# Kernel tuning notes

Measured on AMD Instinct MI355X. Metric: run time of the kernel, lower is better.

## Reference

```python
import jax, jax.numpy as jnp
import numpy as np

B, C, D_IN, D_H, D_OUT = 131072, 16, 256, 1024, 256


def setup_inputs() -> dict:
    key = jax.random.key(0)
    k = jax.random.split(key, 6)
    return {
        "x": jax.random.normal(k[0], (B, D_IN), dtype=jnp.float32),
        "cat_ids": jax.random.randint(k[1], (B,), 0, C, dtype=jnp.int32),
        "W1": jax.random.normal(k[2], (C, D_IN, D_H), dtype=jnp.float32) * (1.0 / np.sqrt(D_IN)),
        "b1": jax.random.normal(k[3], (C, D_H), dtype=jnp.float32) * 0.02,
        "W2": jax.random.normal(k[4], (C, D_H, D_OUT), dtype=jnp.float32) * (1.0 / np.sqrt(D_H)),
        "b2": jax.random.normal(k[5], (C, D_OUT), dtype=jnp.float32) * 0.02,
    }


def _routed_linear(x, cat_ids, W, b):
    # Category-routed linear: out[i] = x[i] @ W[cat_ids[i]] + b[cat_ids[i]].
    # Loop over the small fixed category count (not over tokens); each branch
    # is a dense GEMM masked by the routing assignment. This is equivalent to
    # the original gather -> per-category Linear -> scatter/argsort pattern
    # without materializing per-token weight gathers.
    num_categories = W.shape[0]
    out = jnp.zeros((x.shape[0], W.shape[2]), dtype=x.dtype)
    for c in range(num_categories):
        mask = (cat_ids == c)[:, None]
        out = out + jnp.where(mask, x @ W[c] + b[c], jnp.zeros((), x.dtype))
    return out


def reference(x, cat_ids, W1, b1, W2, b2):
    hidden = jax.nn.relu(_routed_linear(x, cat_ids, W1, b1))
    return _routed_linear(hidden, cat_ids, W2, b2)
```

## Files before the change

kernel.cpp:

```cpp
#include <hip/hip_runtime.h>
#include <hip/hip_bf16.h>

#define BB   131072
#define CC   16
#define DIN  256
#define DH   1024
#define DOUT 256
#define TM   128
#define NHB  16
#define NB   512

typedef __attribute__((ext_vector_type(8))) short bf16x8;
typedef __attribute__((ext_vector_type(4))) short short4v;
typedef __attribute__((ext_vector_type(4))) float f32x4;

__device__ inline unsigned short f2b(float f) {
  union { float f; unsigned u; } v; v.f = f;
  unsigned u = v.u;
  return (unsigned short)((u + 0x7fffu + ((u >> 16) & 1u)) >> 16);
}

__device__ inline void gload_lds16(const void* g, void* l) {
  __builtin_amdgcn_global_load_lds(
      (const __attribute__((address_space(1))) void*)g,
      (__attribute__((address_space(3))) void*)l, 16, 0, 0);
}

#define MFMA16(a, b, c) __builtin_amdgcn_mfma_f32_16x16x32_bf16((a), (b), (c), 0, 0, 0)

__global__ void hist_k(const int* __restrict__ cat, int* __restrict__ blockhist) {
  __shared__ int h[CC];
  const int tid = threadIdx.x;
  if (tid < CC) h[tid] = 0;
  __syncthreads();
  const int i = blockIdx.x * 256 + tid;
  atomicAdd(&h[cat[i]], 1);
  __syncthreads();
  if (tid < CC) blockhist[blockIdx.x * CC + tid] = h[tid];
}

__global__ void offsets2_k(const int* __restrict__ blockhist,
                           int* __restrict__ counts, int* __restrict__ padoff,
                           int* __restrict__ base) {
  __shared__ int part[CC][64];
  __shared__ int pref[CC][64];
  __shared__ int scnt[CC];
  __shared__ int spad[CC + 1];
  const int tid = threadIdx.x;
  const int c = tid >> 6;
  const int g = tid & 63;
  int h[8];
  int s = 0;
#pragma unroll
  for (int i = 0; i < 8; i++) {
    h[i] = blockhist[(g * 8 + i) * CC + c];
    s += h[i];
  }
  part[c][g] = s;
  __syncthreads();
  if (g == 0) {
    int r = 0;
    for (int j = 0; j < 64; j++) { pref[c][j] = r; r += part[c][j]; }
    scnt[c] = r;
  }
  __syncthreads();
  if (tid == 0) {
    int acc = 0;
    for (int c2 = 0; c2 < CC; c2++) {
      spad[c2] = acc;
      padoff[c2] = acc;
      counts[c2] = scnt[c2];
      acc += ((scnt[c2] + TM - 1) / TM) * TM;
    }
    spad[CC] = acc;
    padoff[CC] = acc;
  }
  __syncthreads();
  int run = spad[c] + pref[c][g];
#pragma unroll
  for (int i = 0; i < 8; i++) {
    base[(g * 8 + i) * CC + c] = run;
    run += h[i];
  }
}

__global__ void scatter2_k(const int* __restrict__ cat, const int* __restrict__ base,
                           int* __restrict__ idx) {
  __shared__ int cur[CC];
  const int tid = threadIdx.x;
  if (tid < CC) cur[tid] = base[blockIdx.x * CC + tid];
  __syncthreads();
  const int i = blockIdx.x * 256 + tid;
  const int c = cat[i];
  const int pos = atomicAdd(&cur[c], 1);
  idx[pos] = i;
}

__global__ void conv_w1_k(const float* __restrict__ W1, short* __restrict__ w1b) {
  int t = blockIdx.x * blockDim.x + threadIdx.x;
  int n  = t & 1023;
  int j8 = (t >> 10) & 31;
  int c  = t >> 15;
  const float* src = W1 + (size_t)c * DIN * DH;
  bf16x8 o;
#pragma unroll
  for (int i = 0; i < 8; i++)
    o[i] = (short)f2b(src[(size_t)(j8 * 8 + i) * DH + n]);
  char* dst = (char*)w1b + (size_t)c * 524288
            + (n >> 6) * 32768 + ((n >> 4) & 3) * 8192 + (j8 >> 2) * 1024
            + ((n & 15) + 16 * (j8 & 3)) * 16;
  *(bf16x8*)dst = o;
}

__global__ void conv_w2_k(const float* __restrict__ W2, short* __restrict__ w2b) {
  int t = blockIdx.x * blockDim.x + threadIdx.x;
  int n  = t & 255;
  int j8 = (t >> 8) & 127;
  int c  = t >> 15;
  const float* src = W2 + (size_t)c * DH * DOUT;
  bf16x8 o;
#pragma unroll
  for (int i = 0; i < 8; i++)
    o[i] = (short)f2b(src[(size_t)(j8 * 8 + i) * DOUT + n]);
  char* dst = (char*)w2b + (size_t)c * 524288
            + (j8 >> 3) * 32768 + (n >> 4) * 2048 + ((j8 >> 2) & 1) * 1024
            + ((n & 15) + 16 * (j8 & 3)) * 16;
  *(bf16x8*)dst = o;
}

#define W2OFF  65536
#define HSOFF  131072
#define TKOFF  147456
#define B1OFF  147968
#define B2OFF  152064
#define SMSZ   153088

__launch_bounds__(512, 2)
__global__ void mlp_k(const float* __restrict__ x,
                      const float* __restrict__ b1,
                      const float* __restrict__ b2,
                      const short* __restrict__ w1b,
                      const short* __restrict__ w2b,
                      const int* __restrict__ idx,
                      const int* __restrict__ padoff,
                      const int* __restrict__ counts,
                      float* __restrict__ out) {
  __shared__ __align__(16) char sm[SMSZ];

  const int bhw = blockIdx.x;
  const int wg = (bhw & 7) * 130 + (bhw >> 3);
  const int p = wg * TM;
  const int total = padoff[CC];
  if (p >= total) return;
  int c = 0;
  while (padoff[c + 1] <= p) c++;
  const int cnt = counts[c];
  const int start = p - padoff[c];

  const int tid  = threadIdx.x;
  const int lane = tid & 63;
  const int w    = tid >> 6;
  const int wt   = w >> 1;
  const int wh   = w & 1;
  const int lrow = lane & 15;
  const int lgrp = lane >> 4;

  char*  hsb   = sm + HSOFF;
  int*   toksp = (int*)(sm + TKOFF);
  float* b1s   = (float*)(sm + B1OFF);
  float* b2s   = (float*)(sm + B2OFF);

  {
    const int r = tid >> 2;
    const int q = tid & 3;
    const int pos = start + r;
    int tok = (pos < cnt) ? idx[p + r] : -1;
    if (q == 0) toksp[r] = tok;
    char* tb = sm + (r >> 4) * 8192 + (r & 15) * 16;
    if (tok >= 0) {
      const f32x4* src = (const f32x4*)(x + (size_t)tok * DIN) + q * 16;
#pragma unroll
      for (int t = 0; t < 8; t++) {
        f32x4 v0 = src[2 * t];
        f32x4 v1 = src[2 * t + 1];
        bf16x8 o;
        o[0] = (short)f2b(v0[0]); o[1] = (short)f2b(v0[1]);
        o[2] = (short)f2b(v0[2]); o[3] = (short)f2b(v0[3]);
        o[4] = (short)f2b(v1[0]); o[5] = (short)f2b(v1[1]);
        o[6] = (short)f2b(v1[2]); o[7] = (short)f2b(v1[3]);
        *(bf16x8*)(tb + (2 * q + (t >> 2)) * 1024 + (t & 3) * 256) = o;
      }
    } else {
      bf16x8 z = {0, 0, 0, 0, 0, 0, 0, 0};
#pragma unroll
      for (int t = 0; t < 8; t++)
        *(bf16x8*)(tb + (2 * q + (t >> 2)) * 1024 + (t & 3) * 256) = z;
    }
    if (tid < 256) ((f32x4*)b1s)[tid] = ((const f32x4*)(b1 + (size_t)c * DH))[tid];
    if (tid < 64)  ((f32x4*)b2s)[tid] = ((const f32x4*)(b2 + (size_t)c * DOUT))[tid];
  }
  __syncthreads();

  bf16x8 xf[2][8];
#pragma unroll
  for (int ti = 0; ti < 2; ti++)
#pragma unroll
    for (int ks = 0; ks < 8; ks++)
      xf[ti][ks] = *(const bf16x8*)(sm + (2 * wt + ti) * 8192 + ks * 1024 + lane * 16);
  __syncthreads();

  const char* w1g = (const char*)w1b + (size_t)c * 524288;
  const char* w2g = (const char*)w2b + (size_t)c * 524288;

  auto stage1 = [&](int i) {
    const char* src = w1g + (size_t)i * 32768;
    char* dst = sm + (i & 1) * 32768;
#pragma unroll
    for (int j = 0; j < 4; j++) {
      int chunk = (w * 4 + j) * 1024;
      gload_lds16(src + chunk + lane * 16, dst + chunk);
    }
  };
  auto stage2 = [&](int i) {
    const char* src = w2g + (size_t)i * 32768;
    char* dst = sm + W2OFF + (i & 1) * 32768;
#pragma unroll
    for (int j = 0; j < 4; j++) {
      int chunk = (w * 4 + j) * 1024;
      gload_lds16(src + chunk + lane * 16, dst + chunk);
    }
  };

  stage1(0);
  stage2(0);
  asm volatile("s_waitcnt vmcnt(0)" ::: "memory");
  __syncthreads();

  f32x4 acc2[2][8];
#pragma unroll
  for (int ti = 0; ti < 2; ti++)
#pragma unroll
    for (int ni = 0; ni < 8; ni++)
      acc2[ti][ni] = (f32x4){0.f, 0.f, 0.f, 0.f};

  for (int hb = 0; hb < NHB; hb++) {
    const char* w1c = sm + (hb & 1) * 32768;
    const char* w2c = sm + W2OFF + (hb & 1) * 32768;

    if (hb < NHB - 1) { stage1(hb + 1); stage2(hb + 1); }

    f32x4 acc1[2][2];
#pragma unroll
    for (int ti = 0; ti < 2; ti++)
#pragma unroll
      for (int nj = 0; nj < 2; nj++)
        acc1[ti][nj] = (f32x4){0.f, 0.f, 0.f, 0.f};

#pragma unroll
    for (int ks = 0; ks < 8; ks++) {
      bf16x8 a0 = *(const bf16x8*)(w1c + (2 * wh + 0) * 8192 + ks * 1024 + lane * 16);
      bf16x8 a1 = *(const bf16x8*)(w1c + (2 * wh + 1) * 8192 + ks * 1024 + lane * 16);
      acc1[0][0] = MFMA16(a0, xf[0][ks], acc1[0][0]);
      acc1[1][0] = MFMA16(a0, xf[1][ks], acc1[1][0]);
      acc1[0][1] = MFMA16(a1, xf[0][ks], acc1[0][1]);
      acc1[1][1] = MFMA16(a1, xf[1][ks], acc1[1][1]);
    }

#pragma unroll
    for (int nj = 0; nj < 2; nj++) {
      f32x4 bv = *(const f32x4*)(b1s + hb * 64 + (2 * wh + nj) * 16 + lgrp * 4);
#pragma unroll
      for (int ti = 0; ti < 2; ti++) {
        short4v h;
#pragma unroll
        for (int jj = 0; jj < 4; jj++)
          h[jj] = (short)f2b(fmaxf(acc1[ti][nj][jj] + bv[jj], 0.0f));
        *(short4v*)(hsb + (2 * wt + ti) * 2048 + wh * 1024
                    + (lrow + 16 * (2 * nj + (lgrp >> 1))) * 16 + (lgrp & 1) * 8) = h;
      }
    }
    if (hb < NHB - 1)
      asm volatile("s_waitcnt vmcnt(8) lgkmcnt(0)" ::: "memory");
    else
      asm volatile("s_waitcnt vmcnt(0) lgkmcnt(0)" ::: "memory");
    __builtin_amdgcn_s_barrier();

#pragma unroll
    for (int ks = 0; ks < 2; ks++) {
      bf16x8 hf0 = *(const bf16x8*)(hsb + (2 * wt + 0) * 2048 + ks * 1024 + lane * 16);
      bf16x8 hf1 = *(const bf16x8*)(hsb + (2 * wt + 1) * 2048 + ks * 1024 + lane * 16);
#pragma unroll
      for (int ni = 0; ni < 8; ni++) {
        bf16x8 a2 = *(const bf16x8*)(w2c + (wh * 8 + ni) * 2048 + ks * 1024 + lane * 16);
        acc2[0][ni] = MFMA16(a2, hf0, acc2[0][ni]);
        acc2[1][ni] = MFMA16(a2, hf1, acc2[1][ni]);
      }
    }
    asm volatile("s_waitcnt vmcnt(4) lgkmcnt(0)" ::: "memory");
    __builtin_amdgcn_s_barrier();
  }

#pragma unroll
  for (int ti = 0; ti < 2; ti++) {
    const int tok = toksp[(2 * wt + ti) * 16 + lrow];
    if (tok >= 0) {
#pragma unroll
      for (int ni = 0; ni < 8; ni++) {
        const int n0 = (wh * 8 + ni) * 16 + lgrp * 4;
        f32x4 bv = *(const f32x4*)(b2s + n0);
        f32x4 v = acc2[ti][ni] + bv;
        *(f32x4*)(out + (size_t)tok * DOUT + n0) = v;
      }
    }
  }
}

extern "C" void kernel_launch(void* const* d_in, const int* in_sizes, int n_in,
                              void* d_out, int out_size, void* d_ws, size_t ws_size,
                              hipStream_t stream) {
  (void)in_sizes; (void)n_in; (void)out_size; (void)ws_size;
  const float* x   = (const float*)d_in[0];
  const int*   cat = (const int*)d_in[1];
  const float* W1  = (const float*)d_in[2];
  const float* b1  = (const float*)d_in[3];
  const float* W2  = (const float*)d_in[4];
  const float* b2  = (const float*)d_in[5];
  float* out = (float*)d_out;

  char* ws = (char*)d_ws;
  int* counts    = (int*)(ws);
  int* padoff    = (int*)(ws + 128);
  int* blockhist = (int*)(ws + 4096);
  int* base      = (int*)(ws + 65536);
  int* idx       = (int*)(ws + 131072);
  short* w1b     = (short*)(ws + (1 << 20));
  short* w2b     = (short*)(ws + (1 << 20) + 8388608);

  hist_k<<<NB, 256, 0, stream>>>(cat, blockhist);
  offsets2_k<<<1, 1024, 0, stream>>>(blockhist, counts, padoff, base);
  scatter2_k<<<NB, 256, 0, stream>>>(cat, base, idx);
  conv_w1_k<<<2048, 256, 0, stream>>>(W1, w1b);
  conv_w2_k<<<2048, 256, 0, stream>>>(W2, w2b);

  const int ntiles = BB / TM + CC;
  mlp_k<<<ntiles, 512, 0, stream>>>(x, b1, b2, w1b, w2b, idx, padoff, counts, out);
}
```

Measured before the change: 243.8 us.

## Split hidden-block loop into barrier-separated phases with prefetch-all-then-MFMA and setprio

Restructures each hidden-block iteration into four phases. Each phase first issues all its LDS fragment reads (and one of the global->LDS stage copies), then hits a block barrier, and then runs a dense MFMA burst under raised wave priority. This is a ping-pong style schedule meant to keep waves in lockstep so LDS reads and matrix-core work from different waves interleave better. It adds many extra barriers and more live registers for the prefetched fragments, which risks sync stalls and lower occupancy. The stage1/stage2 prefetches are also spread across phases rather than issued together.

Result: slower. 264.6 us (+8.6%).

```diff
diff --git a/kernel.cpp b/kernel.cpp
--- a/kernel.cpp
+++ b/kernel.cpp
@@ -246,8 +246,7 @@
   for (int hb = 0; hb < NHB; hb++) {
     const char* w1c = sm + (hb & 1) * 32768;
     const char* w2c = sm + W2OFF + (hb & 1) * 32768;
-
-    if (hb < NHB - 1) { stage1(hb + 1); stage2(hb + 1); }
+    const bool notlast = (hb < NHB - 1);
 
     f32x4 acc1[2][2];
 #pragma unroll
@@ -256,48 +255,102 @@
       for (int nj = 0; nj < 2; nj++)
         acc1[ti][nj] = (f32x4){0.f, 0.f, 0.f, 0.f};
 
-#pragma unroll
-    for (int ks = 0; ks < 8; ks++) {
-      bf16x8 a0 = *(const bf16x8*)(w1c + (2 * wh + 0) * 8192 + ks * 1024 + lane * 16);
-      bf16x8 a1 = *(const bf16x8*)(w1c + (2 * wh + 1) * 8192 + ks * 1024 + lane * 16);
-      acc1[0][0] = MFMA16(a0, xf[0][ks], acc1[0][0]);
-      acc1[1][0] = MFMA16(a0, xf[1][ks], acc1[1][0]);
-      acc1[0][1] = MFMA16(a1, xf[0][ks], acc1[0][1]);
-      acc1[1][1] = MFMA16(a1, xf[1][ks], acc1[1][1]);
-    }
-
-#pragma unroll
-    for (int nj = 0; nj < 2; nj++) {
-      f32x4 bv = *(const f32x4*)(b1s + hb * 64 + (2 * wh + nj) * 16 + lgrp * 4);
-#pragma unroll
-      for (int ti = 0; ti < 2; ti++) {
-        short4v h;
-#pragma unroll
-        for (int jj = 0; jj < 4; jj++)
-          h[jj] = (short)f2b(fmaxf(acc1[ti][nj][jj] + bv[jj], 0.0f));
-        *(short4v*)(hsb + (2 * wt + ti) * 2048 + wh * 1024
-                    + (lrow + 16 * (2 * nj + (lgrp >> 1))) * 16 + (lgrp & 1) * 8) = h;
-      }
-    }
-    if (hb < NHB - 1)
-      asm volatile("s_waitcnt vmcnt(8) lgkmcnt(0)" ::: "memory");
-    else
-      asm volatile("s_waitcnt vmcnt(0) lgkmcnt(0)" ::: "memory");
-    __builtin_amdgcn_s_barrier();
-
-#pragma unroll
-    for (int ks = 0; ks < 2; ks++) {
-      bf16x8 hf0 = *(const bf16x8*)(hsb + (2 * wt + 0) * 2048 + ks * 1024 + lane * 16);
-      bf16x8 hf1 = *(const bf16x8*)(hsb + (2 * wt + 1) * 2048 + ks * 1024 + lane * 16);
+    {
+      bf16x8 a[8];
+#pragma unroll
+      for (int ks = 0; ks < 8; ks++)
+        a[ks] = *(const bf16x8*)(w1c + (2 * wh) * 8192 + ks * 1024 + lane * 16);
+      if (notlast) stage1(hb + 1);
+      __builtin_amdgcn_s_barrier();
+      asm volatile("s_waitcnt lgkmcnt(0)" ::: "memory");
+      __builtin_amdgcn_sched_barrier(0);
+      __builtin_amdgcn_s_setprio(1);
+#pragma unroll
+      for (int ks = 0; ks < 8; ks++) {
+        acc1[0][0] = MFMA16(a[ks], xf[0][ks], acc1[0][0]);
+        acc1[1][0] = MFMA16(a[ks], xf[1][ks], acc1[1][0]);
+      }
+      __builtin_amdgcn_s_setprio(0);
+      __builtin_amdgcn_s_barrier();
+    }
+
+    {
+      bf16x8 a[8];
+#pragma unroll
+      for (int ks = 0; ks < 8; ks++)
+        a[ks] = *(const bf16x8*)(w1c + (2 * wh + 1) * 8192 + ks * 1024 + lane * 16);
+      if (notlast) stage2(hb + 1);
+      __builtin_amdgcn_s_barrier();
+      asm volatile("s_waitcnt lgkmcnt(0)" ::: "memory");
+      __builtin_amdgcn_sched_barrier(0);
+      __builtin_amdgcn_s_setprio(1);
+#pragma unroll
+      for (int ks = 0; ks < 8; ks++) {
+        acc1[0][1] = MFMA16(a[ks], xf[0][ks], acc1[0][1]);
+        acc1[1][1] = MFMA16(a[ks], xf[1][ks], acc1[1][1]);
+      }
+      __builtin_amdgcn_s_setprio(0);
+#pragma unroll
+      for (int nj = 0; nj < 2; nj++) {
+        f32x4 bv = *(const f32x4*)(b1s + hb * 64 + (2 * wh + nj) * 16 + lgrp * 4);
+#pragma unroll
+        for (int ti = 0; ti < 2; ti++) {
+          short4v h;
+#pragma unroll
+          for (int jj = 0; jj < 4; jj++)
+            h[jj] = (short)f2b(fmaxf(acc1[ti][nj][jj] + bv[jj], 0.0f));
+          *(short4v*)(hsb + (2 * wt + ti) * 2048 + wh * 1024
+                      + (lrow + 16 * (2 * nj + (lgrp >> 1))) * 16 + (lgrp & 1) * 8) = h;
+        }
+      }
+      if (notlast)
+        asm volatile("s_waitcnt vmcnt(8) lgkmcnt(0)" ::: "memory");
+      else
+        asm volatile("s_waitcnt vmcnt(0) lgkmcnt(0)" ::: "memory");
+      __builtin_amdgcn_s_barrier();
+    }
+
+    {
+      bf16x8 hf0 = *(const bf16x8*)(hsb + (2 * wt + 0) * 2048 + lane * 16);
+      bf16x8 hf1 = *(const bf16x8*)(hsb + (2 * wt + 1) * 2048 + lane * 16);
+      bf16x8 a2[8];
+#pragma unroll
+      for (int ni = 0; ni < 8; ni++)
+        a2[ni] = *(const bf16x8*)(w2c + (wh * 8 + ni) * 2048 + lane * 16);
+      __builtin_amdgcn_s_barrier();
+      asm volatile("s_waitcnt lgkmcnt(0)" ::: "memory");
+      __builtin_amdgcn_sched_barrier(0);
+      __builtin_amdgcn_s_setprio(1);
 #pragma unroll
       for (int ni = 0; ni < 8; ni++) {
-        bf16x8 a2 = *(const bf16x8*)(w2c + (wh * 8 + ni) * 2048 + ks * 1024 + lane * 16);
-        acc2[0][ni] = MFMA16(a2, hf0, acc2[0][ni]);
-        acc2[1][ni] = MFMA16(a2, hf1, acc2[1][ni]);
-      }
-    }
-    asm volatile("s_waitcnt vmcnt(4) lgkmcnt(0)" ::: "memory");
-    __builtin_amdgcn_s_barrier();
+        acc2[0][ni] = MFMA16(a2[ni], hf0, acc2[0][ni]);
+        acc2[1][ni] = MFMA16(a2[ni], hf1, acc2[1][ni]);
+      }
+      __builtin_amdgcn_s_setprio(0);
+      __builtin_amdgcn_s_barrier();
+    }
+
+    {
+      bf16x8 hf0 = *(const bf16x8*)(hsb + (2 * wt + 0) * 2048 + 1024 + lane * 16);
+      bf16x8 hf1 = *(const bf16x8*)(hsb + (2 * wt + 1) * 2048 + 1024 + lane * 16);
+      bf16x8 a2[8];
+#pragma unroll
+      for (int ni = 0; ni < 8; ni++)
+        a2[ni] = *(const bf16x8*)(w2c + (wh * 8 + ni) * 2048 + 1024 + lane * 16);
+      __builtin_amdgcn_s_barrier();
+      asm volatile("s_waitcnt lgkmcnt(0)" ::: "memory");
+      __builtin_amdgcn_sched_barrier(0);
+      __builtin_amdgcn_s_setprio(1);
+#pragma unroll
+      for (int ni = 0; ni < 8; ni++) {
+        acc2[0][ni] = MFMA16(a2[ni], hf0, acc2[0][ni]);
+        acc2[1][ni] = MFMA16(a2[ni], hf1, acc2[1][ni]);
+      }
+      __builtin_amdgcn_s_setprio(0);
+      if (notlast)
+        asm volatile("s_waitcnt vmcnt(4)" ::: "memory");
+      __builtin_amdgcn_s_barrier();
+    }
   }
 
 #pragma unroll
```

## Software-pipeline hidden blocks with halved chunk size and double-buffered hidden tile

Applied to the files above, without the earlier changes.

Halves the hidden-dimension chunk (32 hidden units per step instead of 64) and relayouts W1/W2 bf16 buffers to match, shrinking LDS use. Restructures the loop so the second GEMM for chunk i-1 overlaps with the first GEMM for chunk i, using a double-buffered hidden tile. This removes one barrier per iteration and raises MFMA priority. In exchange there are twice as many iterations and barriers, and each iteration waits on vmcnt(0), so prefetch latency may be exposed.

After: 243.7 us. Within noise of the previous version (-0.0%).

```diff
diff --git a/kernel.cpp b/kernel.cpp
--- a/kernel.cpp
+++ b/kernel.cpp
@@ -7,7 +7,7 @@
 #define DH   1024
 #define DOUT 256
 #define TM   128
-#define NHB  16
+#define NHB  32
 #define NB   512
 
 typedef __attribute__((ext_vector_type(8))) short bf16x8;
@@ -107,7 +107,7 @@
   for (int i = 0; i < 8; i++)
     o[i] = (short)f2b(src[(size_t)(j8 * 8 + i) * DH + n]);
   char* dst = (char*)w1b + (size_t)c * 524288
-            + (n >> 6) * 32768 + ((n >> 4) & 3) * 8192 + (j8 >> 2) * 1024
+            + (n >> 5) * 16384 + ((n >> 4) & 1) * 8192 + (j8 >> 2) * 1024
             + ((n & 15) + 16 * (j8 & 3)) * 16;
   *(bf16x8*)dst = o;
 }
@@ -123,17 +123,17 @@
   for (int i = 0; i < 8; i++)
     o[i] = (short)f2b(src[(size_t)(j8 * 8 + i) * DOUT + n]);
   char* dst = (char*)w2b + (size_t)c * 524288
-            + (j8 >> 3) * 32768 + (n >> 4) * 2048 + ((j8 >> 2) & 1) * 1024
+            + (j8 >> 2) * 16384 + (n >> 4) * 1024
             + ((n & 15) + 16 * (j8 & 3)) * 16;
   *(bf16x8*)dst = o;
 }
 
-#define W2OFF  65536
-#define HSOFF  131072
-#define TKOFF  147456
-#define B1OFF  147968
-#define B2OFF  152064
-#define SMSZ   153088
+#define W2OFF  32768
+#define HSOFF  65536
+#define TKOFF  81920
+#define B1OFF  82432
+#define B2OFF  86528
+#define SMSZ   87552
 
 __launch_bounds__(512, 2)
 __global__ void mlp_k(const float* __restrict__ x,
@@ -213,28 +213,23 @@
   const char* w2g = (const char*)w2b + (size_t)c * 524288;
 
   auto stage1 = [&](int i) {
-    const char* src = w1g + (size_t)i * 32768;
-    char* dst = sm + (i & 1) * 32768;
-#pragma unroll
-    for (int j = 0; j < 4; j++) {
-      int chunk = (w * 4 + j) * 1024;
+    const char* src = w1g + (size_t)i * 16384;
+    char* dst = sm + (i & 1) * 16384;
+#pragma unroll
+    for (int j = 0; j < 2; j++) {
+      int chunk = (w * 2 + j) * 1024;
       gload_lds16(src + chunk + lane * 16, dst + chunk);
     }
   };
   auto stage2 = [&](int i) {
-    const char* src = w2g + (size_t)i * 32768;
-    char* dst = sm + W2OFF + (i & 1) * 32768;
-#pragma unroll
-    for (int j = 0; j < 4; j++) {
-      int chunk = (w * 4 + j) * 1024;
+    const char* src = w2g + (size_t)i * 16384;
+    char* dst = sm + W2OFF + (i & 1) * 16384;
+#pragma unroll
+    for (int j = 0; j < 2; j++) {
+      int chunk = (w * 2 + j) * 1024;
       gload_lds16(src + chunk + lane * 16, dst + chunk);
     }
   };
-
-  stage1(0);
-  stage2(0);
-  asm volatile("s_waitcnt vmcnt(0)" ::: "memory");
-  __syncthreads();
 
   f32x4 acc2[2][8];
 #pragma unroll
@@ -243,61 +238,93 @@
     for (int ni = 0; ni < 8; ni++)
       acc2[ti][ni] = (f32x4){0.f, 0.f, 0.f, 0.f};
 
-  for (int hb = 0; hb < NHB; hb++) {
-    const char* w1c = sm + (hb & 1) * 32768;
-    const char* w2c = sm + W2OFF + (hb & 1) * 32768;
-
-    if (hb < NHB - 1) { stage1(hb + 1); stage2(hb + 1); }
-
-    f32x4 acc1[2][2];
-#pragma unroll
-    for (int ti = 0; ti < 2; ti++)
-#pragma unroll
-      for (int nj = 0; nj < 2; nj++)
-        acc1[ti][nj] = (f32x4){0.f, 0.f, 0.f, 0.f};
-
+  const int hswr = (lrow + 16 * (wh * 2 + (lgrp >> 1))) * 16 + (lgrp & 1) * 8;
+
+  stage1(0);
+  asm volatile("s_waitcnt vmcnt(0)" ::: "memory");
+  __builtin_amdgcn_s_barrier();
+
+  {
+    stage2(0);
+    stage1(1);
+    const char* w1c = sm + wh * 8192;
+    f32x4 p0 = (f32x4){0.f, 0.f, 0.f, 0.f};
+    f32x4 p1 = (f32x4){0.f, 0.f, 0.f, 0.f};
+    __builtin_amdgcn_s_setprio(1);
 #pragma unroll
     for (int ks = 0; ks < 8; ks++) {
-      bf16x8 a0 = *(const bf16x8*)(w1c + (2 * wh + 0) * 8192 + ks * 1024 + lane * 16);
-      bf16x8 a1 = *(const bf16x8*)(w1c + (2 * wh + 1) * 8192 + ks * 1024 + lane * 16);
-      acc1[0][0] = MFMA16(a0, xf[0][ks], acc1[0][0]);
-      acc1[1][0] = MFMA16(a0, xf[1][ks], acc1[1][0]);
-      acc1[0][1] = MFMA16(a1, xf[0][ks], acc1[0][1]);
-      acc1[1][1] = MFMA16(a1, xf[1][ks], acc1[1][1]);
-    }
-
-#pragma unroll
-    for (int nj = 0; nj < 2; nj++) {
-      f32x4 bv = *(const f32x4*)(b1s + hb * 64 + (2 * wh + nj) * 16 + lgrp * 4);
-#pragma unroll
-      for (int ti = 0; ti < 2; ti++) {
-        short4v h;
-#pragma unroll
-        for (int jj = 0; jj < 4; jj++)
-          h[jj] = (short)f2b(fmaxf(acc1[ti][nj][jj] + bv[jj], 0.0f));
-        *(short4v*)(hsb + (2 * wt + ti) * 2048 + wh * 1024
-                    + (lrow + 16 * (2 * nj + (lgrp >> 1))) * 16 + (lgrp & 1) * 8) = h;
-      }
-    }
-    if (hb < NHB - 1)
-      asm volatile("s_waitcnt vmcnt(8) lgkmcnt(0)" ::: "memory");
-    else
-      asm volatile("s_waitcnt vmcnt(0) lgkmcnt(0)" ::: "memory");
+      bf16x8 a = *(const bf16x8*)(w1c + ks * 1024 + lane * 16);
+      p0 = MFMA16(a, xf[0][ks], p0);
+      p1 = MFMA16(a, xf[1][ks], p1);
+    }
+    __builtin_amdgcn_s_setprio(0);
+    f32x4 bv = *(const f32x4*)(b1s + wh * 16 + lgrp * 4);
+    short4v h0, h1;
+#pragma unroll
+    for (int jj = 0; jj < 4; jj++) {
+      h0[jj] = (short)f2b(fmaxf(p0[jj] + bv[jj], 0.0f));
+      h1[jj] = (short)f2b(fmaxf(p1[jj] + bv[jj], 0.0f));
+    }
+    *(short4v*)(hsb + (2 * wt) * 1024 + hswr)     = h0;
+    *(short4v*)(hsb + (2 * wt + 1) * 1024 + hswr) = h1;
+    asm volatile("s_waitcnt vmcnt(0) lgkmcnt(0)" ::: "memory");
     __builtin_amdgcn_s_barrier();
-
-#pragma unroll
-    for (int ks = 0; ks < 2; ks++) {
-      bf16x8 hf0 = *(const bf16x8*)(hsb + (2 * wt + 0) * 2048 + ks * 1024 + lane * 16);
-      bf16x8 hf1 = *(const bf16x8*)(hsb + (2 * wt + 1) * 2048 + ks * 1024 + lane * 16);
-#pragma unroll
-      for (int ni = 0; ni < 8; ni++) {
-        bf16x8 a2 = *(const bf16x8*)(w2c + (wh * 8 + ni) * 2048 + ks * 1024 + lane * 16);
-        acc2[0][ni] = MFMA16(a2, hf0, acc2[0][ni]);
-        acc2[1][ni] = MFMA16(a2, hf1, acc2[1][ni]);
-      }
-    }
-    asm volatile("s_waitcnt vmcnt(4) lgkmcnt(0)" ::: "memory");
+  }
+
+  for (int i = 1; i < NHB; i++) {
+    stage2(i);
+    if (i < NHB - 1) stage1(i + 1);
+
+    const char* hr  = hsb + ((i - 1) & 1) * 8192;
+    const char* w2c = sm + W2OFF + ((i - 1) & 1) * 16384;
+    const char* w1c = sm + (i & 1) * 16384 + wh * 8192;
+
+    bf16x8 hf0 = *(const bf16x8*)(hr + (2 * wt) * 1024 + lane * 16);
+    bf16x8 hf1 = *(const bf16x8*)(hr + (2 * wt + 1) * 1024 + lane * 16);
+
+    __builtin_amdgcn_s_setprio(1);
+#pragma unroll
+    for (int ni = 0; ni < 8; ni++) {
+      bf16x8 a2 = *(const bf16x8*)(w2c + (wh * 8 + ni) * 1024 + lane * 16);
+      acc2[0][ni] = MFMA16(a2, hf0, acc2[0][ni]);
+      acc2[1][ni] = MFMA16(a2, hf1, acc2[1][ni]);
+    }
+    f32x4 p0 = (f32x4){0.f, 0.f, 0.f, 0.f};
+    f32x4 p1 = (f32x4){0.f, 0.f, 0.f, 0.f};
+#pragma unroll
+    for (int ks = 0; ks < 8; ks++) {
+      bf16x8 a = *(const bf16x8*)(w1c + ks * 1024 + lane * 16);
+      p0 = MFMA16(a, xf[0][ks], p0);
+      p1 = MFMA16(a, xf[1][ks], p1);
+    }
+    __builtin_amdgcn_s_setprio(0);
+
+    f32x4 bv = *(const f32x4*)(b1s + i * 32 + wh * 16 + lgrp * 4);
+    short4v h0, h1;
+#pragma unroll
+    for (int jj = 0; jj < 4; jj++) {
+      h0[jj] = (short)f2b(fmaxf(p0[jj] + bv[jj], 0.0f));
+      h1[jj] = (short)f2b(fmaxf(p1[jj] + bv[jj], 0.0f));
+    }
+    char* hw = hsb + (i & 1) * 8192;
+    *(short4v*)(hw + (2 * wt) * 1024 + hswr)     = h0;
+    *(short4v*)(hw + (2 * wt + 1) * 1024 + hswr) = h1;
+
+    asm volatile("s_waitcnt vmcnt(0) lgkmcnt(0)" ::: "memory");
     __builtin_amdgcn_s_barrier();
+  }
+
+  {
+    const char* hr  = hsb + ((NHB - 1) & 1) * 8192;
+    const char* w2c = sm + W2OFF + ((NHB - 1) & 1) * 16384;
+    bf16x8 hf0 = *(const bf16x8*)(hr + (2 * wt) * 1024 + lane * 16);
+    bf16x8 hf1 = *(const bf16x8*)(hr + (2 * wt + 1) * 1024 + lane * 16);
+#pragma unroll
+    for (int ni = 0; ni < 8; ni++) {
+      bf16x8 a2 = *(const bf16x8*)(w2c + (wh * 8 + ni) * 1024 + lane * 16);
+      acc2[0][ni] = MFMA16(a2, hf0, acc2[0][ni]);
+      acc2[1][ni] = MFMA16(a2, hf1, acc2[1][ni]);
+    }
   }
 
 #pragma unroll
```
